# Kernel tuning notes

Hardware: AMD Instinct MI355X
Metric: run time of the kernel (lower is better)

Reference implementation:

```python
import jax, jax.numpy as jnp
import numpy as np

B, S, DIN, H, DOUT, E, SEL = 8, 2048, 512, 512, 512, 262144, 512
N = B * S


def setup_inputs() -> dict:
    key = jax.random.key(0)
    ks = jax.random.split(key, 20)
    inp = {
        "x": jax.random.normal(ks[0], (B, S, DIN), dtype=jnp.float32),
        "edge_index": jax.random.randint(ks[1], (2, E), 0, N, dtype=jnp.int64),
        "selected_idx": jax.random.randint(ks[2], (B, SEL), 0, S, dtype=jnp.int64),
        "edge_label": jax.random.randint(ks[3], (E,), 0, 8, dtype=jnp.int64),
    }
    k = 4
    for l, fin in enumerate([DIN, H, H]):
        inp[f"conv{l}_w1"] = jax.random.normal(ks[k], (2 * fin, H), dtype=jnp.float32) * 0.02; k += 1
        inp[f"conv{l}_b1"] = jnp.full((H,), 0.01, dtype=jnp.float32)
        inp[f"conv{l}_w2"] = jax.random.normal(ks[k], (H, H), dtype=jnp.float32) * 0.02; k += 1
        inp[f"conv{l}_b2"] = jnp.full((H,), 0.01, dtype=jnp.float32)
    inp["ffn_w1"] = jax.random.normal(ks[k], (H, H), dtype=jnp.float32) * 0.02; k += 1
    inp["ffn_b1"] = jnp.full((H,), 0.01, dtype=jnp.float32)
    inp["ffn_w2"] = jax.random.normal(ks[k], (H, DOUT), dtype=jnp.float32) * 0.02; k += 1
    inp["ffn_b2"] = jnp.full((DOUT,), 0.01, dtype=jnp.float32)
    return inp


def _ffw(x, w1, b1, w2, b2):
    # FeedForward: fc2(act_dropout(relu(fc1(x)))), dropout=0 in eval
    return jax.nn.relu(x @ w1 + b1) @ w2 + b2


def reference(x, edge_index, selected_idx, edge_label,
              conv0_w1, conv0_b1, conv0_w2, conv0_b2,
              conv1_w1, conv1_b1, conv1_w2, conv1_b2,
              conv2_w1, conv2_b1, conv2_w2, conv2_b2,
              ffn_w1, ffn_b1, ffn_w2, ffn_b2):
    b, s, d = x.shape
    n = b * s
    h = x.reshape(n, d)
    src, dst = edge_index[0], edge_index[1]  # PyG: x_j = source, x_i = target
    convs = [(conv0_w1, conv0_b1, conv0_w2, conv0_b2),
             (conv1_w1, conv1_b1, conv1_w2, conv1_b2),
             (conv2_w1, conv2_b1, conv2_w2, conv2_b2)]
    for w1, b1, w2, b2 in convs:
        xi = h[dst]                                   # [E, F]
        xj = h[src]
        ef = jnp.concatenate([xi, xj - xi], axis=1)   # [E, 2F]
        m = _ffw(ef, w1, b1, w2, b2)                  # per-edge MLP [E, H]
        agg = jax.ops.segment_max(m, dst, num_segments=n)
        agg = jnp.where(jnp.isneginf(agg), 0.0, agg)  # empty segments -> 0 (PyG fill)
        h = jax.nn.relu(agg)                          # dropout p acts as identity in eval
    h = _ffw(h, ffn_w1, ffn_b1, ffn_w2, ffn_b2)
    out = h.reshape(b, s, -1)                         # [B, S, DOUT]
    idx = jnp.broadcast_to(selected_idx[:, :, None], (b, selected_idx.shape[1], out.shape[-1]))
    return jnp.take_along_axis(out, idx, axis=1)      # [B, SEL, DOUT]
```

## Files before the change

kernel.cpp:

```cpp
#include <hip/hip_runtime.h>
#include <hip/hip_bf16.h>


#define N_NODES 16384
#define EDGES   262144
#define HDIM    512
#define SEQ     2048

typedef __attribute__((ext_vector_type(8))) short short8;
typedef __attribute__((ext_vector_type(8))) _Float16 half8;
typedef __attribute__((ext_vector_type(2))) _Float16 half2v;
typedef __attribute__((ext_vector_type(4))) float f32x4;

__device__ __forceinline__ void gld16(const void* g, void* l) {
    __builtin_amdgcn_global_load_lds(
        (const __attribute__((address_space(1))) void*)g,
        (__attribute__((address_space(3))) void*)l, 16, 0, 0);
}
__device__ __forceinline__ unsigned short f2b(float f) {
    unsigned int x = __float_as_uint(f);
    return (unsigned short)((x + 0x7fffu + ((x >> 16) & 1u)) >> 16);
}
__device__ __forceinline__ unsigned short f2h(float f) {
    _Float16 h = (_Float16)f;
    return __builtin_bit_cast(unsigned short, h);
}
__device__ __forceinline__ unsigned int zpack_h(unsigned int u, unsigned int v) {
    half2v a = __builtin_bit_cast(half2v, u);
    half2v b = __builtin_bit_cast(half2v, v);
    half2v s = a + b;
    half2v z = {(_Float16)0.f, (_Float16)0.f};
    half2v r = __builtin_elementwise_max(s, z);
    return __builtin_bit_cast(unsigned int, r);
}
__device__ __forceinline__ short8 frag_ld(const short* S, int row, int q) {
    int p = q ^ ((row >> 1) & 3);
    return *(const short8*)(S + row * 32 + p * 8);
}
__device__ __forceinline__ void stage_tile(const short* G, int kc, short* S, int t) {
#pragma unroll
    for (int it = 0; it < 2; ++it) {
        int lin = it * 256 + t;
        int row = lin >> 2, p = lin & 3;
        int q = p ^ ((row >> 1) & 3);
        gld16(G + (size_t)row * HDIM + kc + q * 8, S + lin * 8);
    }
}
__device__ __forceinline__ half8 frag64(const short* S, int row, int q) {
    int p = q ^ ((row >> 1) & 7) ^ (row & 1);
    return *(const half8*)(S + row * 64 + p * 8);
}

__global__ __launch_bounds__(256) void hist_kernel(
    const int* __restrict__ dst, int* __restrict__ hist) {
    int idx = blockIdx.x * 256 + threadIdx.x;
    atomicAdd(&hist[dst[idx]], 1);
}
__global__ __launch_bounds__(256) void scan_kernel(
    const int* __restrict__ hist, int* __restrict__ cursor) {
    __shared__ int part[256];
    const int t = threadIdx.x, base = t * 64;
    int sum = 0;
    for (int i = 0; i < 64; ++i) sum += hist[base + i];
    part[t] = sum;
    __syncthreads();
    int run = 0;
    for (int i = 0; i < t; ++i) run += part[i];
    for (int i = 0; i < 64; ++i) {
        int h = hist[base + i];
        cursor[base + i] = run;
        run += h;
    }
}
__global__ __launch_bounds__(256) void scatter_kernel(
    const int* __restrict__ dst, const int* __restrict__ src,
    int* __restrict__ cursor, int* __restrict__ dstS, int* __restrict__ srcS) {
    int idx = blockIdx.x * 256 + threadIdx.x;
    int d = dst[idx];
    int p = atomicAdd(&cursor[d], 1);
    dstS[p] = d;
    srcS[p] = src[idx];
}

__global__ __launch_bounds__(256) void prep_weights_all_kernel(
    const float* __restrict__ w1_0, const float* __restrict__ w2_0,
    const float* __restrict__ w1_1, const float* __restrict__ w2_1,
    const float* __restrict__ w1_2, const float* __restrict__ w2_2,
    short* __restrict__ outbase) {
    __shared__ float tile[32][33];
    const int z = blockIdx.z;
    const int layer = z / 3, which = z % 3;
    const float* w1 = layer == 0 ? w1_0 : (layer == 1 ? w1_1 : w1_2);
    const float* w2 = layer == 0 ? w2_0 : (layer == 1 ? w2_1 : w2_2);
    const int k0 = blockIdx.x * 32, n0 = blockIdx.y * 32;
    const int tx = threadIdx.x, ty = threadIdx.y;
#pragma unroll
    for (int i = 0; i < 4; ++i) {
        int k = k0 + ty + i * 8, n = n0 + tx;
        float v;
        if (which == 0)      v = w1[k * 512 + n] - w1[(k + 512) * 512 + n];
        else if (which == 1) v = w1[(k + 512) * 512 + n];
        else                 v = w2[k * 512 + n];
        tile[ty + i * 8][tx] = v;
    }
    __syncthreads();
    short* out = outbase + (size_t)(layer * 3 + which) * 512 * 512;
#pragma unroll
    for (int i = 0; i < 4; ++i) {
        int n = n0 + ty + i * 8, k = k0 + tx;
        float v = tile[tx][ty + i * 8];
        if (which == 2) {
            int lane = (n & 15) | (((k >> 3) & 3) << 4);
            size_t idx = ((size_t)((n >> 4) * 16 + (k >> 5)) * 64 + lane) * 8 + (k & 7);
            out[idx] = (short)f2h(v);
        } else {
            out[(size_t)n * 512 + k] = (short)f2b(v);
        }
    }
}
__global__ __launch_bounds__(256) void tr_kernel(
    const float* __restrict__ W1, const float* __restrict__ W2,
    short* __restrict__ T1, short* __restrict__ T2) {
    __shared__ float tile[32][33];
    const float* W = blockIdx.z ? W2 : W1;
    short* T = blockIdx.z ? T2 : T1;
    const int k0 = blockIdx.x * 32, n0 = blockIdx.y * 32;
    const int tx = threadIdx.x, ty = threadIdx.y;
#pragma unroll
    for (int i = 0; i < 4; ++i)
        tile[ty + i * 8][tx] = W[(k0 + ty + i * 8) * 512 + n0 + tx];
    __syncthreads();
#pragma unroll
    for (int i = 0; i < 4; ++i)
        T[(size_t)(n0 + ty + i * 8) * 512 + k0 + tx] = (short)f2b(tile[tx][ty + i * 8]);
}
__global__ __launch_bounds__(256) void cvt_bf16_kernel(
    const float* __restrict__ x, short* __restrict__ xb) {
    int idx = blockIdx.x * 256 + threadIdx.x;
    float4 v = ((const float4*)x)[idx];
    uint2 o;
    o.x = (unsigned int)f2b(v.x) | ((unsigned int)f2b(v.y) << 16);
    o.y = (unsigned int)f2b(v.z) | ((unsigned int)f2b(v.w) << 16);
    ((uint2*)xb)[idx] = o;
}

__global__ __launch_bounds__(256, 2) void node_gemm_uv_kernel(
    const short* __restrict__ A, const short* __restrict__ WdT,
    const short* __restrict__ w1bT, const float* __restrict__ b1,
    short* __restrict__ U, short* __restrict__ V) {
    __shared__ short As[2][128 * 32];
    __shared__ short Bu[2][128 * 32];
    __shared__ short Bv[2][128 * 32];
    const int t = threadIdx.x;
    const int m0 = blockIdx.x * 128, n0 = blockIdx.y * 128;
    const int w = t >> 6, l = t & 63;
    const int wm = (w & 1) * 64, wn = (w >> 1) * 64;
    const short* Ag = A + (size_t)m0 * HDIM;
    const short* Ug = WdT + (size_t)n0 * HDIM;
    const short* Vg = w1bT + (size_t)n0 * HDIM;
    f32x4 aU[4][4] = {}, aV[4][4] = {};
    stage_tile(Ag, 0, As[0], t);
    stage_tile(Ug, 0, Bu[0], t);
    stage_tile(Vg, 0, Bv[0], t);
#pragma unroll
    for (int hh = 0; hh < 16; ++hh) {
        if (hh < 15) {
            const int kc1 = (hh + 1) * 32;
            stage_tile(Ag, kc1, As[(hh + 1) & 1], t);
            stage_tile(Ug, kc1, Bu[(hh + 1) & 1], t);
            stage_tile(Vg, kc1, Bv[(hh + 1) & 1], t);
            asm volatile("s_waitcnt vmcnt(6)" ::: "memory");
        } else {
            asm volatile("s_waitcnt vmcnt(0)" ::: "memory");
        }
        __builtin_amdgcn_s_barrier();
        asm volatile("" ::: "memory");
        const short* Ab = As[hh & 1];
        const short* Bub = Bu[hh & 1];
        const short* Bvb = Bv[hh & 1];
        short8 a[4], bu[4], bv[4];
#pragma unroll
        for (int mt = 0; mt < 4; ++mt) a[mt] = frag_ld(Ab, wm + mt * 16 + (l & 15), l >> 4);
#pragma unroll
        for (int nt = 0; nt < 4; ++nt) {
            bu[nt] = frag_ld(Bub, wn + nt * 16 + (l & 15), l >> 4);
            bv[nt] = frag_ld(Bvb, wn + nt * 16 + (l & 15), l >> 4);
        }
#pragma unroll
        for (int mt = 0; mt < 4; ++mt)
#pragma unroll
            for (int nt = 0; nt < 4; ++nt) {
                aU[mt][nt] = __builtin_amdgcn_mfma_f32_16x16x32_bf16(a[mt], bu[nt], aU[mt][nt], 0, 0, 0);
                aV[mt][nt] = __builtin_amdgcn_mfma_f32_16x16x32_bf16(a[mt], bv[nt], aV[mt][nt], 0, 0, 0);
            }
        asm volatile("" ::: "memory");
        __builtin_amdgcn_s_barrier();
    }
#pragma unroll
    for (int mt = 0; mt < 4; ++mt) {
        int m = m0 + wm + mt * 16 + (l >> 4) * 4;
#pragma unroll
        for (int nt = 0; nt < 4; ++nt) {
            int n = n0 + wn + nt * 16 + (l & 15);
            float bv = b1[n];
#pragma unroll
            for (int r = 0; r < 4; ++r) {
                U[(size_t)(m + r) * HDIM + n] = (short)f2h(aU[mt][nt][r] + bv);
                V[(size_t)(m + r) * HDIM + n] = (short)f2h(aV[mt][nt][r]);
            }
        }
    }
}

__device__ __forceinline__ unsigned int fkey(float m) {
    unsigned int b = __float_as_uint(m);
    return ((int)b < 0) ? ~b : (b | 0x80000000u);
}
__device__ __forceinline__ void kflush(unsigned int* K, int d, int col, float m) {
    atomicMax(K + (((size_t)d) << 9) + col, fkey(m));
}
__global__ __launch_bounds__(256, 3) void edge_mfma_kernel(
    const short* __restrict__ U, const short* __restrict__ V,
    const short* __restrict__ W2f, const int* __restrict__ srcS,
    const int* __restrict__ dstS, unsigned int* __restrict__ K) {
    __shared__ short As[64 * 64];
    __shared__ unsigned int ktile[16 * 256];
    __shared__ int sdst[64], ssrc[64];
    const int t = threadIdx.x;
    const int L  = blockIdx.x;
    const int g  = (L >> 4) * 8 + (L & 7);
    const int nh = (L >> 3) & 1;
    const int e0 = g * 64, n0 = nh * 256;
    if (t < 64) { sdst[t] = dstS[e0 + t]; ssrc[t] = srcS[e0 + t]; }
    __syncthreads();
    const int w = t >> 6, l = t & 63;
    const int wnb = w * 64;
    const int lm = l & 15;
    const int arow = t >> 2, s0 = (t & 3) * 2;
    const int perm = ((arow >> 1) & 7) ^ (arow & 1);
    const int p0 = s0 ^ perm, p1 = (s0 + 1) ^ perm;
    const short* up = U + (((size_t)sdst[arow]) << 9) + s0 * 8;
    const short* vp = V + (((size_t)ssrc[arow]) << 9) + s0 * 8;
    const short* bp = W2f + (size_t)((n0 + wnb) >> 4) * 8192 + (size_t)l * 8;
    unsigned int* As_u = (unsigned int*)As;
    f32x4 acc[4][4] = {};
    half8 bc[4], bn[4];
    uint4 pu0, pu1, pv0, pv1;
#pragma unroll
    for (int nt = 0; nt < 4; ++nt) bc[nt] = *(const half8*)(bp + nt * 8192);
    pu0 = *(const uint4*)(up);      pu1 = *(const uint4*)(up + 8);
    pv0 = *(const uint4*)(vp);      pv1 = *(const uint4*)(vp + 8);
    {
        uint4 z0, z1;
        z0.x = zpack_h(pu0.x, pv0.x); z0.y = zpack_h(pu0.y, pv0.y);
        z0.z = zpack_h(pu0.z, pv0.z); z0.w = zpack_h(pu0.w, pv0.w);
        z1.x = zpack_h(pu1.x, pv1.x); z1.y = zpack_h(pu1.y, pv1.y);
        z1.z = zpack_h(pu1.z, pv1.z); z1.w = zpack_h(pu1.w, pv1.w);
        *(uint4*)(As_u + arow * 32 + p0 * 4) = z0;
        *(uint4*)(As_u + arow * 32 + p1 * 4) = z1;
    }
    pu0 = *(const uint4*)(up + 64); pu1 = *(const uint4*)(up + 72);
    pv0 = *(const uint4*)(vp + 64); pv1 = *(const uint4*)(vp + 72);
    asm volatile("s_waitcnt lgkmcnt(0)" ::: "memory");
    __builtin_amdgcn_s_barrier();
    asm volatile("" ::: "memory");
#pragma unroll
    for (int j = 0; j < 8; ++j) {
        const int h1 = 2 * j + 1;
#pragma unroll
        for (int nt = 0; nt < 4; ++nt)
            bn[nt] = *(const half8*)(bp + nt * 8192 + h1 * 512);
        __builtin_amdgcn_s_setprio(1);
#pragma unroll
        for (int mt = 0; mt < 4; ++mt) {
            half8 a = frag64(As, mt * 16 + lm, (l >> 4));
#pragma unroll
            for (int nt = 0; nt < 4; ++nt)
                acc[mt][nt] = __builtin_amdgcn_mfma_f32_16x16x32_f16(a, bc[nt], acc[mt][nt], 0, 0, 0);
        }
        __builtin_amdgcn_s_setprio(0);
        if (j < 7) {
#pragma unroll
            for (int nt = 0; nt < 4; ++nt)
                bc[nt] = *(const half8*)(bp + nt * 8192 + (h1 + 1) * 512);
        }
        __builtin_amdgcn_s_setprio(1);
#pragma unroll
        for (int mt = 0; mt < 4; ++mt) {
            half8 a = frag64(As, mt * 16 + lm, 4 + (l >> 4));
#pragma unroll
            for (int nt = 0; nt < 4; ++nt)
                acc[mt][nt] = __builtin_amdgcn_mfma_f32_16x16x32_f16(a, bn[nt], acc[mt][nt], 0, 0, 0);
        }
        __builtin_amdgcn_s_setprio(0);
        asm volatile("s_waitcnt lgkmcnt(0)" ::: "memory");
        __builtin_amdgcn_s_barrier();
        asm volatile("" ::: "memory");
        if (j < 7) {
            uint4 z0, z1;
            z0.x = zpack_h(pu0.x, pv0.x); z0.y = zpack_h(pu0.y, pv0.y);
            z0.z = zpack_h(pu0.z, pv0.z); z0.w = zpack_h(pu0.w, pv0.w);
            z1.x = zpack_h(pu1.x, pv1.x); z1.y = zpack_h(pu1.y, pv1.y);
            z1.z = zpack_h(pu1.z, pv1.z); z1.w = zpack_h(pu1.w, pv1.w);
            *(uint4*)(As_u + arow * 32 + p0 * 4) = z0;
            *(uint4*)(As_u + arow * 32 + p1 * 4) = z1;
            if (j < 6) {
                const int kn = (j + 2) * 64;
                pu0 = *(const uint4*)(up + kn);      pu1 = *(const uint4*)(up + kn + 8);
                pv0 = *(const uint4*)(vp + kn);      pv1 = *(const uint4*)(vp + kn + 8);
            }
            asm volatile("s_waitcnt lgkmcnt(0)" ::: "memory");
            __builtin_amdgcn_s_barrier();
            asm volatile("" ::: "memory");
        }
    }
    const int dbase = sdst[0];
    const int drange = sdst[63] - dbase + 1;
    if (drange <= 16) {
#pragma unroll
        for (int i = 0; i < 16; ++i) ktile[i * 256 + t] = 0u;
        __syncthreads();
#pragma unroll
        for (int mt = 0; mt < 4; ++mt) {
            int base = mt * 16 + (l >> 4) * 4;
            int d0 = sdst[base], d1 = sdst[base + 1], d2 = sdst[base + 2], d3 = sdst[base + 3];
            int r0 = d0 - dbase, r1 = d1 - dbase, r2 = d2 - dbase, r3 = d3 - dbase;
#pragma unroll
            for (int nt = 0; nt < 4; ++nt) {
                int colb = wnb + nt * 16 + lm;
                f32x4 a = acc[mt][nt];
                float m = a[0];
                if (d1 == d0) m = fmaxf(m, a[1]);
                else { atomicMax(ktile + r0 * 256 + colb, fkey(m)); m = a[1]; }
                if (d2 == d1) m = fmaxf(m, a[2]);
                else { atomicMax(ktile + r1 * 256 + colb, fkey(m)); m = a[2]; }
                if (d3 == d2) m = fmaxf(m, a[3]);
                else { atomicMax(ktile + r2 * 256 + colb, fkey(m)); m = a[3]; }
                atomicMax(ktile + r3 * 256 + colb, fkey(m));
            }
        }
        __syncthreads();
#pragma unroll 4
        for (int r = 0; r < 16; ++r) {
            if (r < drange) {
                unsigned int kv = ktile[r * 256 + t];
                if (kv) atomicMax(K + (((size_t)(dbase + r)) << 9) + n0 + t, kv);
            }
        }
    } else {
#pragma unroll
        for (int mt = 0; mt < 4; ++mt) {
            int base = mt * 16 + (l >> 4) * 4;
            int d0 = sdst[base], d1 = sdst[base + 1], d2 = sdst[base + 2], d3 = sdst[base + 3];
#pragma unroll
            for (int nt = 0; nt < 4; ++nt) {
                int col = n0 + wnb + nt * 16 + lm;
                f32x4 a = acc[mt][nt];
                float m = a[0];
                if (d1 == d0) m = fmaxf(m, a[1]); else { kflush(K, d0, col, m); m = a[1]; }
                if (d2 == d1) m = fmaxf(m, a[2]); else { kflush(K, d1, col, m); m = a[2]; }
                if (d3 == d2) m = fmaxf(m, a[3]); else { kflush(K, d2, col, m); m = a[3]; }
                kflush(K, d3, col, m);
            }
        }
    }
}

__global__ __launch_bounds__(256) void decode_kernel(
    unsigned int* __restrict__ K, const float* __restrict__ b2,
    short* __restrict__ hb) {
    int idx = blockIdx.x * 256 + threadIdx.x;
    uint2 k = ((uint2*)K)[idx];
    uint2 zz = {0u, 0u};
    ((uint2*)K)[idx] = zz;
    int c = (idx << 1) & (HDIM - 1);
    float v0 = 0.f, v1 = 0.f;
    if (k.x != 0u) {
        unsigned int b = (k.x & 0x80000000u) ? (k.x ^ 0x80000000u) : ~k.x;
        v0 = __uint_as_float(b) + b2[c];
    }
    if (k.y != 0u) {
        unsigned int b = (k.y & 0x80000000u) ? (k.y ^ 0x80000000u) : ~k.y;
        v1 = __uint_as_float(b) + b2[c + 1];
    }
    unsigned int o = (unsigned int)f2b(fmaxf(v0, 0.f))
                   | ((unsigned int)f2b(fmaxf(v1, 0.f)) << 16);
    ((unsigned int*)hb)[idx] = o;
}

__global__ __launch_bounds__(256) void ffn_gemm_kernel(
    const short* __restrict__ A, const int* __restrict__ sel,
    const short* __restrict__ Wt, const float* __restrict__ bias,
    short* __restrict__ Cb, float* __restrict__ Cf, int relu) {
    __shared__ short As[64 * 32];
    __shared__ short Bs[128 * 32];
    const int t = threadIdx.x;
    const int m0 = blockIdx.x * 64, n0 = blockIdx.y * 128;
    const int w = t >> 6, l = t & 63;
    const int wm = (w & 1) * 32, wn = (w >> 1) * 64;
    const int srow = t >> 2, sp = t & 3;
    const int sq = sp ^ ((srow >> 1) & 3);
    const short* ap;
    if (sel) {
        int gr = m0 + srow;
        ap = A + (((size_t)((gr >> 9) * SEQ + sel[gr])) << 9);
    } else {
        ap = A + (size_t)(m0 + srow) * HDIM;
    }
    f32x4 acc[2][4] = {};
    for (int kc = 0; kc < HDIM; kc += 32) {
        gld16(ap + kc + sq * 8, As + t * 8);
        stage_tile(Wt + (size_t)n0 * HDIM, kc, Bs, t);
        __syncthreads();
        short8 a[2], b[4];
#pragma unroll
        for (int mt = 0; mt < 2; ++mt) a[mt] = frag_ld(As, wm + mt * 16 + (l & 15), l >> 4);
#pragma unroll
        for (int nt = 0; nt < 4; ++nt) b[nt] = frag_ld(Bs, wn + nt * 16 + (l & 15), l >> 4);
#pragma unroll
        for (int mt = 0; mt < 2; ++mt)
#pragma unroll
            for (int nt = 0; nt < 4; ++nt)
                acc[mt][nt] = __builtin_amdgcn_mfma_f32_16x16x32_bf16(a[mt], b[nt], acc[mt][nt], 0, 0, 0);
        __syncthreads();
    }
#pragma unroll
    for (int mt = 0; mt < 2; ++mt) {
        int m = m0 + wm + mt * 16 + (l >> 4) * 4;
#pragma unroll
        for (int nt = 0; nt < 4; ++nt) {
            int n = n0 + wn + nt * 16 + (l & 15);
            float bv = bias[n];
#pragma unroll
            for (int r = 0; r < 4; ++r) {
                float v = acc[mt][nt][r] + bv;
                if (relu) v = fmaxf(v, 0.f);
                if (Cf) Cf[(size_t)(m + r) * HDIM + n] = v;
                else    Cb[(size_t)(m + r) * HDIM + n] = (short)f2b(v);
            }
        }
    }
}

extern "C" void kernel_launch(void* const* d_in, const int* in_sizes, int n_in,
                              void* d_out, int out_size, void* d_ws, size_t ws_size,
                              hipStream_t stream) {
    const float* x   = (const float*)d_in[0];
    const int*   ei  = (const int*)d_in[1];
    const int*   sel = (const int*)d_in[2];
    const int*   src = ei;
    const int*   dst = ei + EDGES;
    const float* cw1[3] = {(const float*)d_in[4],  (const float*)d_in[8],  (const float*)d_in[12]};
    const float* cb1[3] = {(const float*)d_in[5],  (const float*)d_in[9],  (const float*)d_in[13]};
    const float* cw2[3] = {(const float*)d_in[6],  (const float*)d_in[10], (const float*)d_in[14]};
    const float* cb2[3] = {(const float*)d_in[7],  (const float*)d_in[11], (const float*)d_in[15]};
    const float* fw1 = (const float*)d_in[16];
    const float* fb1 = (const float*)d_in[17];
    const float* fw2 = (const float*)d_in[18];
    const float* fb2 = (const float*)d_in[19];
    float* out = (float*)d_out;

    const size_t MB = 1024 * 1024;
    char* p = (char*)d_ws;
    unsigned int* keys = (unsigned int*)p;
    short* U    = (short*)(p + 32 * MB);
    short* V    = (short*)(p + 48 * MB);
    short* hb   = (short*)(p + 64 * MB);
    short* Wall = (short*)(p + 80 * MB);
    short* fw1T = Wall + 9 * 512 * 512;
    short* fw2T = fw1T + 512 * 512;
    int*   dstS = (int*)(p + 86 * MB);
    int*   srcS = (int*)(p + 87 * MB);
    int*   hist = (int*)(p + 88 * MB);
    int*   curs = hist + N_NODES;
    short* t1b  = (short*)(p + 89 * MB);

    (void)hipMemsetAsync(hist, 0, N_NODES * sizeof(int), stream);
    hist_kernel<<<EDGES / 256, 256, 0, stream>>>(dst, hist);
    scan_kernel<<<1, 256, 0, stream>>>(hist, curs);
    scatter_kernel<<<EDGES / 256, 256, 0, stream>>>(dst, src, curs, dstS, srcS);

    cvt_bf16_kernel<<<8192, 256, 0, stream>>>(x, hb);
    tr_kernel<<<dim3(16, 16, 2), dim3(32, 8), 0, stream>>>(fw1, fw2, fw1T, fw2T);
    prep_weights_all_kernel<<<dim3(16, 16, 9), dim3(32, 8), 0, stream>>>(
        cw1[0], cw2[0], cw1[1], cw2[1], cw1[2], cw2[2], Wall);
    (void)hipMemsetAsync(keys, 0, 32 * MB, stream);

    for (int l = 0; l < 3; ++l) {
        short* WdT  = Wall + (size_t)(l * 3 + 0) * 512 * 512;
        short* w1bT = Wall + (size_t)(l * 3 + 1) * 512 * 512;
        short* W2f  = Wall + (size_t)(l * 3 + 2) * 512 * 512;
        node_gemm_uv_kernel<<<dim3(128, 4), 256, 0, stream>>>(hb, WdT, w1bT, cb1[l], U, V);
        edge_mfma_kernel<<<8192, 256, 0, stream>>>(U, V, W2f, srcS, dstS, keys);
        decode_kernel<<<(N_NODES * HDIM / 2) / 256, 256, 0, stream>>>(keys, cb2[l], hb);
    }

    ffn_gemm_kernel<<<dim3(64, 4), 256, 0, stream>>>(hb, sel, fw1T, fb1, t1b, nullptr, 1);
    ffn_gemm_kernel<<<dim3(64, 4), 256, 0, stream>>>(t1b, nullptr, fw2T, fb2, nullptr, out, 0);
}
```

Measured before the change: 723.0 us.

## Load node-GEMM weight fragments directly from pre-swizzled global layout into registers

The U/V node-GEMM weights are now stored in the same MFMA-fragment-swizzled layout already used for W2. Each wave loads its B fragments straight from global memory into registers with a double buffer, instead of staging them through LDS. This drops two of the three LDS tiles, leaves one barrier per k-step, and adds s_setprio around the MFMA blocks to interleave the loads. The cost is more global traffic per wave, since weights are no longer shared across waves through LDS, and higher register pressure at two blocks per SIMD occupancy.

```diff
diff --git a/kernel.cpp b/kernel.cpp
--- a/kernel.cpp
+++ b/kernel.cpp
@@ -109,13 +109,9 @@
     for (int i = 0; i < 4; ++i) {
         int n = n0 + ty + i * 8, k = k0 + tx;
         float v = tile[tx][ty + i * 8];
-        if (which == 2) {
-            int lane = (n & 15) | (((k >> 3) & 3) << 4);
-            size_t idx = ((size_t)((n >> 4) * 16 + (k >> 5)) * 64 + lane) * 8 + (k & 7);
-            out[idx] = (short)f2h(v);
-        } else {
-            out[(size_t)n * 512 + k] = (short)f2b(v);
-        }
+        int lane = (n & 15) | (((k >> 3) & 3) << 4);
+        size_t idx = ((size_t)((n >> 4) * 16 + (k >> 5)) * 64 + lane) * 8 + (k & 7);
+        out[idx] = (short)(which == 2 ? f2h(v) : f2b(v));
     }
 }
 __global__ __launch_bounds__(256) void tr_kernel(
@@ -145,56 +141,64 @@
 }
 
 __global__ __launch_bounds__(256, 2) void node_gemm_uv_kernel(
-    const short* __restrict__ A, const short* __restrict__ WdT,
-    const short* __restrict__ w1bT, const float* __restrict__ b1,
+    const short* __restrict__ A, const short* __restrict__ WdF,
+    const short* __restrict__ w1bF, const float* __restrict__ b1,
     short* __restrict__ U, short* __restrict__ V) {
     __shared__ short As[2][128 * 32];
-    __shared__ short Bu[2][128 * 32];
-    __shared__ short Bv[2][128 * 32];
     const int t = threadIdx.x;
     const int m0 = blockIdx.x * 128, n0 = blockIdx.y * 128;
     const int w = t >> 6, l = t & 63;
     const int wm = (w & 1) * 64, wn = (w >> 1) * 64;
     const short* Ag = A + (size_t)m0 * HDIM;
-    const short* Ug = WdT + (size_t)n0 * HDIM;
-    const short* Vg = w1bT + (size_t)n0 * HDIM;
+    const short* bpU = WdF + (size_t)((n0 + wn) >> 4) * 8192 + (size_t)l * 8;
+    const short* bpV = w1bF + (size_t)((n0 + wn) >> 4) * 8192 + (size_t)l * 8;
     f32x4 aU[4][4] = {}, aV[4][4] = {};
+    short8 bu2[2][4], bv2[2][4];
     stage_tile(Ag, 0, As[0], t);
-    stage_tile(Ug, 0, Bu[0], t);
-    stage_tile(Vg, 0, Bv[0], t);
+#pragma unroll
+    for (int nt = 0; nt < 4; ++nt) bu2[0][nt] = *(const short8*)(bpU + nt * 8192);
+#pragma unroll
+    for (int nt = 0; nt < 4; ++nt) bv2[0][nt] = *(const short8*)(bpV + nt * 8192);
+    asm volatile("s_waitcnt vmcnt(8)" ::: "memory");
+    __builtin_amdgcn_s_barrier();
+    asm volatile("" ::: "memory");
 #pragma unroll
     for (int hh = 0; hh < 16; ++hh) {
+        short8 a[4];
+#pragma unroll
+        for (int mt = 0; mt < 4; ++mt)
+            a[mt] = frag_ld(As[hh & 1], wm + mt * 16 + (l & 15), l >> 4);
         if (hh < 15) {
-            const int kc1 = (hh + 1) * 32;
-            stage_tile(Ag, kc1, As[(hh + 1) & 1], t);
-            stage_tile(Ug, kc1, Bu[(hh + 1) & 1], t);
-            stage_tile(Vg, kc1, Bv[(hh + 1) & 1], t);
-            asm volatile("s_waitcnt vmcnt(6)" ::: "memory");
-        } else {
-            asm volatile("s_waitcnt vmcnt(0)" ::: "memory");
-        }
-        __builtin_amdgcn_s_barrier();
-        asm volatile("" ::: "memory");
-        const short* Ab = As[hh & 1];
-        const short* Bub = Bu[hh & 1];
-        const short* Bvb = Bv[hh & 1];
-        short8 a[4], bu[4], bv[4];
-#pragma unroll
-        for (int mt = 0; mt < 4; ++mt) a[mt] = frag_ld(Ab, wm + mt * 16 + (l & 15), l >> 4);
-#pragma unroll
-        for (int nt = 0; nt < 4; ++nt) {
-            bu[nt] = frag_ld(Bub, wn + nt * 16 + (l & 15), l >> 4);
-            bv[nt] = frag_ld(Bvb, wn + nt * 16 + (l & 15), l >> 4);
-        }
+#pragma unroll
+            for (int nt = 0; nt < 4; ++nt)
+                bu2[(hh + 1) & 1][nt] = *(const short8*)(bpU + nt * 8192 + (hh + 1) * 512);
+            stage_tile(Ag, (hh + 1) * 32, As[(hh + 1) & 1], t);
+            asm volatile("" ::: "memory");
+        }
+        __builtin_amdgcn_s_setprio(1);
 #pragma unroll
         for (int mt = 0; mt < 4; ++mt)
 #pragma unroll
-            for (int nt = 0; nt < 4; ++nt) {
-                aU[mt][nt] = __builtin_amdgcn_mfma_f32_16x16x32_bf16(a[mt], bu[nt], aU[mt][nt], 0, 0, 0);
-                aV[mt][nt] = __builtin_amdgcn_mfma_f32_16x16x32_bf16(a[mt], bv[nt], aV[mt][nt], 0, 0, 0);
-            }
-        asm volatile("" ::: "memory");
-        __builtin_amdgcn_s_barrier();
+            for (int nt = 0; nt < 4; ++nt)
+                aU[mt][nt] = __builtin_amdgcn_mfma_f32_16x16x32_bf16(a[mt], bu2[hh & 1][nt], aU[mt][nt], 0, 0, 0);
+        __builtin_amdgcn_s_setprio(0);
+        if (hh < 15) {
+#pragma unroll
+            for (int nt = 0; nt < 4; ++nt)
+                bv2[(hh + 1) & 1][nt] = *(const short8*)(bpV + nt * 8192 + (hh + 1) * 512);
+        }
+        __builtin_amdgcn_s_setprio(1);
+#pragma unroll
+        for (int mt = 0; mt < 4; ++mt)
+#pragma unroll
+            for (int nt = 0; nt < 4; ++nt)
+                aV[mt][nt] = __builtin_amdgcn_mfma_f32_16x16x32_bf16(a[mt], bv2[hh & 1][nt], aV[mt][nt], 0, 0, 0);
+        __builtin_amdgcn_s_setprio(0);
+        if (hh < 15) {
+            asm volatile("s_waitcnt vmcnt(4) lgkmcnt(0)" ::: "memory");
+            __builtin_amdgcn_s_barrier();
+            asm volatile("" ::: "memory");
+        }
     }
 #pragma unroll
     for (int mt = 0; mt < 4; ++mt) {
@@ -487,10 +491,10 @@
     (void)hipMemsetAsync(keys, 0, 32 * MB, stream);
 
     for (int l = 0; l < 3; ++l) {
-        short* WdT  = Wall + (size_t)(l * 3 + 0) * 512 * 512;
-        short* w1bT = Wall + (size_t)(l * 3 + 1) * 512 * 512;
+        short* WdF  = Wall + (size_t)(l * 3 + 0) * 512 * 512;
+        short* w1bF = Wall + (size_t)(l * 3 + 1) * 512 * 512;
         short* W2f  = Wall + (size_t)(l * 3 + 2) * 512 * 512;
-        node_gemm_uv_kernel<<<dim3(128, 4), 256, 0, stream>>>(hb, WdT, w1bT, cb1[l], U, V);
+        node_gemm_uv_kernel<<<dim3(128, 4), 256, 0, stream>>>(hb, WdF, w1bF, cb1[l], U, V);
         edge_mfma_kernel<<<8192, 256, 0, stream>>>(U, V, W2f, srcS, dstS, keys);
         decode_kernel<<<(N_NODES * HDIM / 2) / 256, 256, 0, stream>>>(keys, cb2[l], hb);
     }
```

New measurement: 717.2 us. No clear change (-0.8%).
